# Optimization experiments

Measured on AMD Instinct MI355X. Metric: run time of the kernel, lower is better.

Reference implementation:

```python
import jax, jax.numpy as jnp
import numpy as np

E = 1024
H = 16
DH = E // H
EPS = 1e-8
GRAM_W = 1.5


def _gram_scores(q, k1, k2):
    # q: [BH, L, D], k1/k2: [BH, S, D] -> [BH, L, S]
    ll = jnp.sum(q * q, -1)[:, :, None]          # [BH, L, 1]
    vv = jnp.sum(k1 * k1, -1)[:, None, :]        # [BH, 1, S]
    aa = jnp.sum(k2 * k2, -1)[:, None, :]
    va = jnp.sum(k1 * k2, -1)[:, None, :]
    lv = jnp.einsum('bld,bsd->bls', q, k1)
    la = jnp.einsum('bld,bsd->bls', q, k2)
    det = ll * (vv * aa - va * va) - lv * (lv * aa - la * va) + la * (lv * va - la * vv)
    return -jnp.sqrt(jnp.clip(det, EPS, None))


def setup_inputs() -> dict:
    key = jax.random.key(0)
    ks = jax.random.split(key, 20)
    L, B, S = 512, 4, 1024
    inp = {
        'query': jax.random.normal(ks[0], (L, B, E), jnp.float32),
        'mod1': jax.random.normal(ks[1], (S, B, E), jnp.float32),
        'mod2': jax.random.normal(ks[2], (S, B, E), jnp.float32),
    }
    # Linear params stored as [in, out] (y = x @ W + b), 8 linears
    names = ['q', 'k1', 'k2', 'v1', 'v2', 'g1', 'g2', 'o']
    for i, n in enumerate(names):
        inp[n + '_w'] = jax.random.normal(ks[3 + 2 * i], (E, E), jnp.float32) * 0.02
        inp[n + '_b'] = jax.random.normal(ks[4 + 2 * i], (E,), jnp.float32) * 0.02
    return inp


def reference(query, mod1, mod2,
              q_w, q_b, k1_w, k1_b, k2_w, k2_b, v1_w, v1_b, v2_w, v2_b,
              g1_w, g1_b, g2_w, g2_b, o_w, o_b):
    L, B, _ = query.shape
    S = mod1.shape[0]
    scaling = DH ** -0.5

    def lin(x, w, b):
        return x @ w + b

    def split_heads(x, n):  # [n, B, E] -> [B*H, n, DH]
        return x.reshape(n, B * H, DH).transpose(1, 0, 2)

    q = split_heads(lin(query, q_w, q_b) * scaling, L)
    k1 = split_heads(lin(mod1, k1_w, k1_b), S)
    k2 = split_heads(lin(mod2, k2_w, k2_b), S)
    v1 = split_heads(lin(mod1, v1_w, v1_b), S)
    v2 = split_heads(lin(mod2, v2_w, v2_b), S)

    w1 = jnp.einsum('bld,bsd->bls', q, k1)
    w2 = jnp.einsum('bld,bsd->bls', q, k2)
    gram = _gram_scores(q, k1, k2)
    logits = GRAM_W * gram + w1 + w2          # [BH, L, S]
    attn = jax.nn.softmax(logits, axis=-1)

    def merge_heads(x):  # [B*H, L, DH] -> [L, B, E]
        return x.transpose(1, 0, 2).reshape(L, B, E)

    out1 = merge_heads(jnp.einsum('bls,bsd->bld', attn, v1))
    out2 = merge_heads(jnp.einsum('bls,bsd->bld', attn, v2))
    gate1 = jax.nn.sigmoid(lin(query, g1_w, g1_b))
    gate2 = jax.nn.sigmoid(lin(query, g2_w, g2_b))
    attn_output = lin((out1 * gate1 + out2 * gate2) / 2.0, o_w, o_b)
    avg_weights = attn.reshape(B, H, L, S).mean(axis=1)
    return attn_output, avg_weights
```

## Files before the change

kernel.cpp:

```cpp
#include <hip/hip_runtime.h>
#include <cstddef>
#include <cstdint>

typedef unsigned short ushort_t;
typedef unsigned int uint_t;
typedef __attribute__((ext_vector_type(8))) short short8;
typedef __attribute__((ext_vector_type(4))) float f32x4;

#define EDIM 1024
#define NHEAD 16
#define HDIM 64
#define NB 4
#define LQ 512
#define SK 1024
#define BHD 64

__device__ __forceinline__ ushort_t f2b(float f) {
    uint_t u = __float_as_uint(f);
    return (ushort_t)((u + 0x7fffu + ((u >> 16) & 1u)) >> 16);
}
__device__ __forceinline__ float b2f(ushort_t b) {
    return __uint_as_float(((uint_t)b) << 16);
}

__device__ __forceinline__ void gload_lds16(const void* g, void* l) {
    __builtin_amdgcn_global_load_lds((const __attribute__((address_space(1))) void*)g,
                                     (__attribute__((address_space(3))) void*)l, 16, 0, 0);
}

struct MegaArgs {
    const ushort_t *qx, *m1h, *m1l, *m2h, *m2l;
    const ushort_t *Wqg, *Wkv1, *Wkv2, *Wk1l, *Wk2l;
    const float *q_b, *k1_b, *k2_b, *v1_b, *v2_b, *g1_b, *g2_b;
    float *K1f, *K2f;
    ushort_t *V1b, *V2b, *Qb, *G1b, *G2b;
};

__global__ __launch_bounds__(256, 2)
void mega_gemm(MegaArgs a)
{
    __shared__ ushort_t As[128 * 64];
    __shared__ ushort_t Bs[128 * 64];
    const int tid = threadIdx.x;
    const int wave = tid >> 6, lane = tid & 63;
    const int ln = lane & 15, lq = lane >> 4;
    const int wm = wave & 1, wn = wave >> 1;
    const int cswz = (lane & 7) ^ ((lane >> 3) & 7);
    const int mrl = lane >> 3;

    const int id = blockIdx.x;
    const ushort_t *A, *Al, *B, *Bl;
    const float* bias;
    int npass, row0, col0, kind;
    if (id < 512) {
        kind = id >> 8;
        const int t = id & 255;
        col0 = (t & 7) * 128; row0 = (t >> 3) * 128; npass = 3;
        A = kind ? a.m2h : a.m1h;  Al = kind ? a.m2l : a.m1l;
        B = kind ? a.Wkv2 : a.Wkv1; Bl = kind ? a.Wk2l : a.Wk1l;
        bias = kind ? a.k2_b : a.k1_b;
    } else if (id < 1024) {
        int t = id - 512; kind = 2 + (t >> 8); t &= 255;
        col0 = (t & 7) * 128; row0 = (t >> 3) * 128; npass = 1;
        A = (kind == 2) ? a.m1h : a.m2h; Al = A;
        B = ((kind == 2) ? a.Wkv1 : a.Wkv2) + (size_t)1024 * 1024; Bl = B;
        bias = (kind == 2) ? a.v1_b : a.v2_b;
    } else {
        const int t = id - 1024; kind = 4;
        const int c = t % 24, rr = t / 24;
        col0 = c * 128; row0 = rr * 128; npass = 1;
        A = a.qx; Al = A; B = a.Wqg; Bl = B;
        const int seg = c >> 3;
        bias = (seg == 0) ? a.q_b : ((seg == 1) ? a.g1_b : a.g2_b);
    }

    f32x4 zero = {0.f, 0.f, 0.f, 0.f};
    f32x4 acc[4][4];
#pragma unroll
    for (int i = 0; i < 4; ++i)
#pragma unroll
        for (int j = 0; j < 4; ++j) acc[i][j] = zero;

    for (int pp = 0; pp < npass; ++pp) {
        const ushort_t* Ab = (pp == 2) ? Al : A;
        const ushort_t* Bb = (pp == 1) ? Bl : B;
        for (int kk = 0; kk < 1024; kk += 64) {
            __syncthreads();
#pragma unroll
            for (int j = 0; j < 4; ++j) {
                const int mr = (wave * 4 + j) * 8 + mrl;
                gload_lds16(Ab + (size_t)(row0 + mr) * 1024 + kk + cswz * 8,
                            (void*)(As + (wave * 4 + j) * 512));
                gload_lds16(Bb + (size_t)(col0 + mr) * 1024 + kk + cswz * 8,
                            (void*)(Bs + (wave * 4 + j) * 512));
            }
            __syncthreads();
#pragma unroll
            for (int sub = 0; sub < 2; ++sub) {
                short8 af[4], bfv[4];
#pragma unroll
                for (int i = 0; i < 4; ++i) {
                    const int ml = wm * 64 + i * 16 + ln;
                    af[i] = *(const short8*)(As + ml * 64 + (((sub * 4 + lq) ^ (ml & 7)) * 8));
                    const int nl = wn * 64 + i * 16 + ln;
                    bfv[i] = *(const short8*)(Bs + nl * 64 + (((sub * 4 + lq) ^ (nl & 7)) * 8));
                }
#pragma unroll
                for (int i = 0; i < 4; ++i)
#pragma unroll
                    for (int j = 0; j < 4; ++j)
                        acc[i][j] = __builtin_amdgcn_mfma_f32_16x16x32_bf16(af[i], bfv[j], acc[i][j], 0, 0, 0);
            }
        }
    }

#pragma unroll
    for (int i = 0; i < 4; ++i) {
#pragma unroll
        for (int r = 0; r < 4; ++r) {
            const int row = row0 + wm * 64 + i * 16 + lq * 4 + r;
#pragma unroll
            for (int j = 0; j < 4; ++j) {
                const int col = col0 + wn * 64 + j * 16 + ln;
                const int lc = col & 1023;
                float v = acc[i][j][r] + bias[lc];
                if (kind <= 1) {
                    const int s = row >> 2, b = row & 3, h = lc >> 6, d = lc & 63;
                    float* Y = kind ? a.K2f : a.K1f;
                    Y[(((size_t)(b * 16 + h)) * 1024 + s) * 64 + d] = v;
                } else if (kind <= 3) {
                    const int s = row >> 2, b = row & 3, h = lc >> 6, d = lc & 63;
                    ushort_t* Y = (kind == 2) ? a.V1b : a.V2b;
                    Y[(((size_t)(b * 16 + h)) * 1024 + s) * 64 + d] = f2b(v);
                } else {
                    const int seg = col >> 10;
                    if (seg == 0) {
                        v *= 0.125f;
                        const int s = row >> 2, b = row & 3, h = lc >> 6, d = lc & 63;
                        a.Qb[(((size_t)(b * 16 + h)) * 512 + s) * 64 + d] = f2b(v);
                    } else {
                        v = 1.0f / (1.0f + __expf(-v));
                        ushort_t* Y = (seg == 1) ? a.G1b : a.G2b;
                        Y[(size_t)row * 1024 + lc] = f2b(v);
                    }
                }
            }
        }
    }
}

struct CastArgs {
    const float* q; const float* m1; const float* m2;
    ushort_t* qx; ushort_t* m1h; ushort_t* m1l; ushort_t* m2h; ushort_t* m2l;
    const float* wsrc[8];
    ushort_t* whi[8];
    ushort_t* wlo[8];
};

__global__ __launch_bounds__(256)
void casts_kernel(CastArgs a)
{
    __shared__ float T[64][65];
    const int id = blockIdx.x;
    const int tid = threadIdx.x;
    if (id < 1024) {
        const size_t i = ((size_t)id * 256 + tid) * 8;
        float4 x = *(const float4*)(a.q + i);
        float4 y = *(const float4*)(a.q + i + 4);
        ushort_t o[8] = {f2b(x.x), f2b(x.y), f2b(x.z), f2b(x.w), f2b(y.x), f2b(y.y), f2b(y.z), f2b(y.w)};
        *(uint4*)( (void*)(a.qx + i) ) = *(const uint4*)o;
    } else if (id < 5120) {
        const int t = id - 1024;
        const int which = t >> 11;
        const float* x = which ? a.m2 : a.m1;
        ushort_t* yh = which ? a.m2h : a.m1h;
        ushort_t* yl = which ? a.m2l : a.m1l;
        const size_t i = ((size_t)(t & 2047) * 256 + tid) * 8;
        float v[8];
        *(float4*)v = *(const float4*)(x + i);
        *(float4*)(v + 4) = *(const float4*)(x + i + 4);
        ushort_t oh[8], ol[8];
#pragma unroll
        for (int k = 0; k < 8; ++k) {
            oh[k] = f2b(v[k]);
            ol[k] = f2b(v[k] - b2f(oh[k]));
        }
        *(uint4*)( (void*)(yh + i) ) = *(const uint4*)oh;
        *(uint4*)( (void*)(yl + i) ) = *(const uint4*)ol;
    } else {
        const int t = id - 5120;
        const int z = t >> 8, x = t & 15, y = (t >> 4) & 15;
        const float* W = a.wsrc[z];
        ushort_t* Th = a.whi[z];
        ushort_t* Tl = a.wlo[z];
        const int k0 = x * 64, n0 = y * 64;
        const int r = tid >> 2, cg = (tid & 3) * 16;
#pragma unroll
        for (int u = 0; u < 4; ++u) {
            float4 v = *(const float4*)(W + (size_t)(k0 + r) * 1024 + n0 + cg + u * 4);
            T[r][cg + u * 4 + 0] = v.x; T[r][cg + u * 4 + 1] = v.y;
            T[r][cg + u * 4 + 2] = v.z; T[r][cg + u * 4 + 3] = v.w;
        }
        __syncthreads();
        ushort_t oh[16], ol[16];
#pragma unroll
        for (int u = 0; u < 16; ++u) {
            float v = T[cg + u][r];
            oh[u] = f2b(v);
            ol[u] = f2b(v - b2f(oh[u]));
        }
        ushort_t* dh = Th + (size_t)(n0 + r) * 1024 + k0 + cg;
        *(uint4*)( (void*)dh ) = *(const uint4*)oh;
        *(uint4*)( (void*)(dh + 8) ) = *(const uint4*)(oh + 8);
        if (Tl) {
            ushort_t* dl = Tl + (size_t)(n0 + r) * 1024 + k0 + cg;
            *(uint4*)( (void*)dl ) = *(const uint4*)ol;
            *(uint4*)( (void*)(dl + 8) ) = *(const uint4*)(ol + 8);
        }
    }
}

__global__ __launch_bounds__(256)
void prep_kernel(const float* __restrict__ K1f, const float* __restrict__ K2f,
                 ushort_t* __restrict__ K1b, ushort_t* __restrict__ K2b,
                 float* __restrict__ vv, float* __restrict__ aa, float* __restrict__ va,
                 const ushort_t* __restrict__ Qb, float* __restrict__ ll,
                 const ushort_t* __restrict__ V1b, const ushort_t* __restrict__ V2b,
                 ushort_t* __restrict__ V1t, ushort_t* __restrict__ V2t)
{
    __shared__ float T[64][65];
    const int id = blockIdx.x;
    const int tid = threadIdx.x;
    const int wave = tid >> 6, lane = tid & 63;
    if (id < 16384) {
        const int row = id * 4 + wave;
        const float x1 = K1f[(size_t)row * 64 + lane];
        const float x2 = K2f[(size_t)row * 64 + lane];
        K1b[(size_t)row * 64 + lane] = f2b(x1);
        K2b[(size_t)row * 64 + lane] = f2b(x2);
        float s1 = x1 * x1, s2 = x2 * x2, s3 = x1 * x2;
#pragma unroll
        for (int o = 1; o < 64; o <<= 1) {
            s1 += __shfl_xor(s1, o);
            s2 += __shfl_xor(s2, o);
            s3 += __shfl_xor(s3, o);
        }
        if (lane == 0) { vv[row] = s1; aa[row] = s2; va[row] = s3; }
    } else if (id < 24576) {
        const int row = (id - 16384) * 4 + wave;
        const float x = b2f(Qb[(size_t)row * 64 + lane]);
        float s = x * x;
#pragma unroll
        for (int o = 1; o < 64; o <<= 1) s += __shfl_xor(s, o);
        if (lane == 0) ll[row] = s;
    } else {
        const int t = id - 24576;
        const int z = t >> 10, bh = (t >> 4) & 63, s0 = (t & 15) * 64;
        const ushort_t* S = z ? V2b : V1b;
        ushort_t* D = z ? V2t : V1t;
        const int r = tid >> 2, cg = (tid & 3) * 16;
        ushort_t buf[16];
        const ushort_t* sp = S + ((size_t)bh * 1024 + s0 + r) * 64 + cg;
        *(uint4*)buf = *(const uint4*)sp;
        *(uint4*)(buf + 8) = *(const uint4*)(sp + 8);
#pragma unroll
        for (int u = 0; u < 16; ++u) T[r][cg + u] = b2f(buf[u]);
        __syncthreads();
        ushort_t o[16];
#pragma unroll
        for (int u = 0; u < 16; ++u) o[u] = f2b(T[cg + u][r]);
        ushort_t* d = D + ((size_t)bh * 64 + r) * 1024 + s0 + cg;
        *(uint4*)( (void*)d ) = *(const uint4*)o;
        *(uint4*)( (void*)(d + 8) ) = *(const uint4*)(o + 8);
    }
}

__global__ __launch_bounds__(512, 1)
void flash_attn(const ushort_t* __restrict__ Qb, const ushort_t* __restrict__ K1b,
                const ushort_t* __restrict__ K2b, const ushort_t* __restrict__ V1t,
                const ushort_t* __restrict__ V2t, const float* __restrict__ ll,
                const float* __restrict__ vv, const float* __restrict__ aa,
                const float* __restrict__ va, const ushort_t* __restrict__ G1,
                const ushort_t* __restrict__ G2, ushort_t* __restrict__ attn,
                ushort_t* __restrict__ tmpb)
{
    __shared__ ushort_t Qs[128 * 64];
    __shared__ ushort_t K1s[128 * 64];
    __shared__ ushort_t K2s[128 * 64];
    __shared__ ushort_t V1s[64 * 128];
    __shared__ ushort_t V2s[64 * 128];
    __shared__ ushort_t Ps[128 * 128];
    __shared__ float vvS[1024], aaS[1024], vaS[1024];
    __shared__ float llS[128], mRow[128], sRow[128];
    __shared__ float redM[256], redS[256];

    const int tid = threadIdx.x;
    const int wave = tid >> 6, lane = tid & 63;
    const int ln = lane & 15, lq = lane >> 4;
    const int wm = wave >> 1, wn = wave & 1;
    const int l0 = blockIdx.x * 128;
    const int bh = blockIdx.y;
    const int bq = bh >> 4, h = bh & 15;

    for (int u = tid; u < 1024; u += 512) {
        vvS[u] = vv[(size_t)bh * 1024 + u];
        aaS[u] = aa[(size_t)bh * 1024 + u];
        vaS[u] = va[(size_t)bh * 1024 + u];
    }
    if (tid < 128) {
        llS[tid] = ll[(size_t)bh * 512 + l0 + tid];
        mRow[tid] = -3.4e38f;
        sRow[tid] = 0.f;
    }
#pragma unroll
    for (int c = 0; c < 2; ++c) {
        const int row = wave * 16 + c * 8 + (lane >> 3);
        const int ch = (lane & 7) ^ (row & 7);
        gload_lds16(Qb + ((size_t)bh * 512 + l0 + row) * 64 + ch * 8,
                    (void*)(Qs + (wave * 16 + c * 8) * 64));
    }
    __syncthreads();

    f32x4 zero = {0.f, 0.f, 0.f, 0.f};

    for (int st = 0; st < 8; ++st) {
        const int s0 = st * 128;
        __syncthreads();
#pragma unroll
        for (int c = 0; c < 2; ++c) {
            const int row = wave * 16 + c * 8 + (lane >> 3);
            const int ch = (lane & 7) ^ (row & 7);
            gload_lds16(K1b + ((size_t)bh * 1024 + s0 + row) * 64 + ch * 8,
                        (void*)(K1s + (wave * 16 + c * 8) * 64));
            gload_lds16(K2b + ((size_t)bh * 1024 + s0 + row) * 64 + ch * 8,
                        (void*)(K2s + (wave * 16 + c * 8) * 64));
        }
        __syncthreads();

        f32x4 lv[2][4], la[2][4];
#pragma unroll
        for (int i = 0; i < 2; ++i)
#pragma unroll
            for (int j = 0; j < 4; ++j) { lv[i][j] = zero; la[i][j] = zero; }
#pragma unroll
        for (int sub = 0; sub < 2; ++sub) {
            short8 qf[2], k1f[4], k2f[4];
#pragma unroll
            for (int i = 0; i < 2; ++i) {
                const int ml = wm * 32 + i * 16 + ln;
                qf[i] = *(const short8*)(Qs + ml * 64 + (((sub * 4 + lq) ^ (ml & 7)) * 8));
            }
#pragma unroll
            for (int j = 0; j < 4; ++j) {
                const int nl = wn * 64 + j * 16 + ln;
                k1f[j] = *(const short8*)(K1s + nl * 64 + (((sub * 4 + lq) ^ (nl & 7)) * 8));
                k2f[j] = *(const short8*)(K2s + nl * 64 + (((sub * 4 + lq) ^ (nl & 7)) * 8));
            }
#pragma unroll
            for (int i = 0; i < 2; ++i)
#pragma unroll
                for (int j = 0; j < 4; ++j) {
                    lv[i][j] = __builtin_amdgcn_mfma_f32_16x16x32_bf16(qf[i], k1f[j], lv[i][j], 0, 0, 0);
                    la[i][j] = __builtin_amdgcn_mfma_f32_16x16x32_bf16(qf[i], k2f[j], la[i][j], 0, 0, 0);
                }
        }
#pragma unroll
        for (int i = 0; i < 2; ++i)
#pragma unroll
            for (int j = 0; j < 4; ++j) {
                const int s_loc = wn * 64 + j * 16 + ln;
                const float VV = vvS[s0 + s_loc], AA = aaS[s0 + s_loc], VA = vaS[s0 + s_loc];
#pragma unroll
                for (int r = 0; r < 4; ++r) {
                    const float LL = llS[wm * 32 + i * 16 + lq * 4 + r];
                    const float LV = lv[i][j][r], LA = la[i][j][r];
                    float det = LL * (VV * AA - VA * VA) - LV * (LV * AA - LA * VA) + LA * (LV * VA - LA * VV);
                    det = fmaxf(det, 1e-8f);
                    lv[i][j][r] = LV + LA - 1.5f * sqrtf(det);
                }
            }
#pragma unroll
        for (int i = 0; i < 2; ++i)
#pragma unroll
            for (int r = 0; r < 4; ++r) {
                float m = fmaxf(fmaxf(lv[i][0][r], lv[i][1][r]), fmaxf(lv[i][2][r], lv[i][3][r]));
#pragma unroll
                for (int o = 1; o < 16; o <<= 1) m = fmaxf(m, __shfl_xor(m, o));
                if (ln == 0) redM[wn * 128 + wm * 32 + i * 16 + lq * 4 + r] = m;
            }
        __syncthreads();
        if (tid < 128) {
            const float mo = mRow[tid];
            const float mn = fmaxf(mo, fmaxf(redM[tid], redM[128 + tid]));
            sRow[tid] *= __expf(mo - mn);
            mRow[tid] = mn;
        }
        __syncthreads();
#pragma unroll
        for (int i = 0; i < 2; ++i)
#pragma unroll
            for (int r = 0; r < 4; ++r) {
                const float mr = mRow[wm * 32 + i * 16 + lq * 4 + r];
                float e = __expf(lv[i][0][r] - mr) + __expf(lv[i][1][r] - mr)
                        + __expf(lv[i][2][r] - mr) + __expf(lv[i][3][r] - mr);
#pragma unroll
                for (int o = 1; o < 16; o <<= 1) e += __shfl_xor(e, o);
                if (ln == 0) redS[wn * 128 + wm * 32 + i * 16 + lq * 4 + r] = e;
            }
        __syncthreads();
        if (tid < 128) sRow[tid] += redS[tid] + redS[128 + tid];
    }
    __syncthreads();
    if (tid < 128) sRow[tid] = 1.0f / sRow[tid];

    f32x4 o1[4], o2[4];
#pragma unroll
    for (int j = 0; j < 4; ++j) { o1[j] = zero; o2[j] = zero; }

    for (int st = 0; st < 8; ++st) {
        const int s0 = st * 128;
        __syncthreads();
#pragma unroll
        for (int c = 0; c < 2; ++c) {
            const int row = wave * 16 + c * 8 + (lane >> 3);
            const int ch = (lane & 7) ^ (row & 7);
            gload_lds16(K1b + ((size_t)bh * 1024 + s0 + row) * 64 + ch * 8,
                        (void*)(K1s + (wave * 16 + c * 8) * 64));
            gload_lds16(K2b + ((size_t)bh * 1024 + s0 + row) * 64 + ch * 8,
                        (void*)(K2s + (wave * 16 + c * 8) * 64));
        }
#pragma unroll
        for (int c = 0; c < 2; ++c) {
            const int dr = wave * 8 + c * 4 + (lane >> 4);
            const int ch = (lane & 15) ^ (dr & 7);
            gload_lds16(V1t + ((size_t)bh * 64 + dr) * 1024 + s0 + ch * 8,
                        (void*)(V1s + (wave * 8 + c * 4) * 128));
            gload_lds16(V2t + ((size_t)bh * 64 + dr) * 1024 + s0 + ch * 8,
                        (void*)(V2s + (wave * 8 + c * 4) * 128));
        }
        __syncthreads();

        f32x4 lv[2][4], la[2][4];
#pragma unroll
        for (int i = 0; i < 2; ++i)
#pragma unroll
            for (int j = 0; j < 4; ++j) { lv[i][j] = zero; la[i][j] = zero; }
#pragma unroll
        for (int sub = 0; sub < 2; ++sub) {
            short8 qf[2], k1f[4], k2f[4];
#pragma unroll
            for (int i = 0; i < 2; ++i) {
                const int ml = wm * 32 + i * 16 + ln;
                qf[i] = *(const short8*)(Qs + ml * 64 + (((sub * 4 + lq) ^ (ml & 7)) * 8));
            }
#pragma unroll
            for (int j = 0; j < 4; ++j) {
                const int nl = wn * 64 + j * 16 + ln;
                k1f[j] = *(const short8*)(K1s + nl * 64 + (((sub * 4 + lq) ^ (nl & 7)) * 8));
                k2f[j] = *(const short8*)(K2s + nl * 64 + (((sub * 4 + lq) ^ (nl & 7)) * 8));
            }
#pragma unroll
            for (int i = 0; i < 2; ++i)
#pragma unroll
                for (int j = 0; j < 4; ++j) {
                    lv[i][j] = __builtin_amdgcn_mfma_f32_16x16x32_bf16(qf[i], k1f[j], lv[i][j], 0, 0, 0);
                    la[i][j] = __builtin_amdgcn_mfma_f32_16x16x32_bf16(qf[i], k2f[j], la[i][j], 0, 0, 0);
                }
        }
#pragma unroll
        for (int i = 0; i < 2; ++i)
#pragma unroll
            for (int j = 0; j < 4; ++j) {
                const int s_loc = wn * 64 + j * 16 + ln;
                const float VV = vvS[s0 + s_loc], AA = aaS[s0 + s_loc], VA = vaS[s0 + s_loc];
#pragma unroll
                for (int r = 0; r < 4; ++r) {
                    const int l_loc = wm * 32 + i * 16 + lq * 4 + r;
                    const float LL = llS[l_loc];
                    const float LV = lv[i][j][r], LA = la[i][j][r];
                    float det = LL * (VV * AA - VA * VA) - LV * (LV * AA - LA * VA) + LA * (LV * VA - LA * VV);
                    det = fmaxf(det, 1e-8f);
                    const float lg = LV + LA - 1.5f * sqrtf(det);
                    const float p = __expf(lg - mRow[l_loc]) * sRow[l_loc];
                    Ps[l_loc * 128 + (((s_loc >> 3) ^ (l_loc & 7)) * 8) + (s_loc & 7)] = f2b(p);
                }
            }
        __syncthreads();
#pragma unroll
        for (int it = 0; it < 4; ++it) {
            const int l = it * 32 + (tid >> 4);
            const int c = tid & 15;
            uint4 val = *(const uint4*)(Ps + l * 128 + ((c ^ (l & 7)) * 8));
            *(uint4*)( (void*)(attn + ((size_t)bh * 512 + l0 + l) * 1024 + s0 + c * 8) ) = val;
        }
#pragma unroll
        for (int kt = 0; kt < 4; ++kt) {
            const int lA = wave * 16 + ln;
            short8 pf = *(const short8*)(Ps + lA * 128 + (((kt * 4 + lq) ^ (lA & 7)) * 8));
#pragma unroll
            for (int j = 0; j < 4; ++j) {
                const int d = j * 16 + ln;
                short8 v1f = *(const short8*)(V1s + d * 128 + (((kt * 4 + lq) ^ (d & 7)) * 8));
                short8 v2f = *(const short8*)(V2s + d * 128 + (((kt * 4 + lq) ^ (d & 7)) * 8));
                o1[j] = __builtin_amdgcn_mfma_f32_16x16x32_bf16(pf, v1f, o1[j], 0, 0, 0);
                o2[j] = __builtin_amdgcn_mfma_f32_16x16x32_bf16(pf, v2f, o2[j], 0, 0, 0);
            }
        }
    }
#pragma unroll
    for (int j = 0; j < 4; ++j)
#pragma unroll
        for (int r = 0; r < 4; ++r) {
            const int l = l0 + wave * 16 + lq * 4 + r;
            const int d = j * 16 + ln;
            const size_t addr = ((size_t)l * 4 + bq) * 1024 + h * 64 + d;
            const float v = 0.5f * (o1[j][r] * b2f(G1[addr]) + o2[j][r] * b2f(G2[addr]));
            tmpb[addr] = f2b(v);
        }
}

__global__ __launch_bounds__(256)
void head_avg_kernel(const ushort_t* __restrict__ attn, float* __restrict__ outv)
{
    const int idx = blockIdx.x * 256 + threadIdx.x;
    const int s8 = idx & 127;
    const int l = (idx >> 7) & 511;
    const int b = idx >> 16;
    float acc[8] = {};
#pragma unroll
    for (int h = 0; h < 16; ++h) {
        const ushort_t* p = attn + (((size_t)(b * 16 + h) * 512 + l)) * 1024 + s8 * 8;
        uint4 u = *(const uint4*)p;
        const uint_t uu[4] = {u.x, u.y, u.z, u.w};
#pragma unroll
        for (int q = 0; q < 4; ++q) {
            acc[2 * q]     += __uint_as_float((uu[q] & 0xffffu) << 16);
            acc[2 * q + 1] += __uint_as_float(uu[q] & 0xffff0000u);
        }
    }
    float* d = outv + (size_t)idx * 8;
    float4 o1 = {acc[0] * 0.0625f, acc[1] * 0.0625f, acc[2] * 0.0625f, acc[3] * 0.0625f};
    float4 o2 = {acc[4] * 0.0625f, acc[5] * 0.0625f, acc[6] * 0.0625f, acc[7] * 0.0625f};
    *(float4*)d = o1;
    *(float4*)(d + 4) = o2;
}

__global__ __launch_bounds__(256, 2)
void gemm_o64(const ushort_t* __restrict__ A, const ushort_t* __restrict__ B,
              const float* __restrict__ bias, float* __restrict__ Y)
{
    __shared__ ushort_t As[64 * 64];
    __shared__ ushort_t Bs[128 * 64];
    const int tid = threadIdx.x;
    const int wave = tid >> 6, lane = tid & 63;
    const int ln = lane & 15, lq = lane >> 4;
    const int row0 = blockIdx.y * 64, col0 = blockIdx.x * 128;
    const int wm = wave & 1, wn = wave >> 1;
    const int cswz = (lane & 7) ^ ((lane >> 3) & 7);
    const int mrl = lane >> 3;

    f32x4 zero = {0.f, 0.f, 0.f, 0.f};
    f32x4 acc[2][4];
#pragma unroll
    for (int i = 0; i < 2; ++i)
#pragma unroll
        for (int j = 0; j < 4; ++j) acc[i][j] = zero;

    for (int kk = 0; kk < 1024; kk += 64) {
        __syncthreads();
#pragma unroll
        for (int j = 0; j < 2; ++j) {
            const int mr = (wave * 2 + j) * 8 + mrl;
            gload_lds16(A + (size_t)(row0 + mr) * 1024 + kk + cswz * 8,
                        (void*)(As + (wave * 2 + j) * 512));
        }
#pragma unroll
        for (int j = 0; j < 4; ++j) {
            const int mr = (wave * 4 + j) * 8 + mrl;
            gload_lds16(B + (size_t)(col0 + mr) * 1024 + kk + cswz * 8,
                        (void*)(Bs + (wave * 4 + j) * 512));
        }
        __syncthreads();
#pragma unroll
        for (int sub = 0; sub < 2; ++sub) {
            short8 af[2], bfv[4];
#pragma unroll
            for (int i = 0; i < 2; ++i) {
                const int ml = wm * 32 + i * 16 + ln;
                af[i] = *(const short8*)(As + ml * 64 + (((sub * 4 + lq) ^ (ml & 7)) * 8));
            }
#pragma unroll
            for (int j = 0; j < 4; ++j) {
                const int nl = wn * 64 + j * 16 + ln;
                bfv[j] = *(const short8*)(Bs + nl * 64 + (((sub * 4 + lq) ^ (nl & 7)) * 8));
            }
#pragma unroll
            for (int i = 0; i < 2; ++i)
#pragma unroll
                for (int j = 0; j < 4; ++j)
                    acc[i][j] = __builtin_amdgcn_mfma_f32_16x16x32_bf16(af[i], bfv[j], acc[i][j], 0, 0, 0);
        }
    }

#pragma unroll
    for (int i = 0; i < 2; ++i) {
#pragma unroll
        for (int r = 0; r < 4; ++r) {
            const int row = row0 + wm * 32 + i * 16 + lq * 4 + r;
#pragma unroll
            for (int j = 0; j < 4; ++j) {
                const int col = col0 + wn * 64 + j * 16 + ln;
                Y[(size_t)row * 1024 + col] = acc[i][j][r] + bias[col];
            }
        }
    }
}

extern "C" void kernel_launch(void* const* d_in, const int* in_sizes, int n_in,
                              void* d_out, int out_size, void* d_ws, size_t ws_size,
                              hipStream_t stream)
{
    const float* query = (const float*)d_in[0];
    const float* mod1  = (const float*)d_in[1];
    const float* mod2  = (const float*)d_in[2];
    const float* q_w  = (const float*)d_in[3];  const float* q_b  = (const float*)d_in[4];
    const float* k1_w = (const float*)d_in[5];  const float* k1_b = (const float*)d_in[6];
    const float* k2_w = (const float*)d_in[7];  const float* k2_b = (const float*)d_in[8];
    const float* v1_w = (const float*)d_in[9];  const float* v1_b = (const float*)d_in[10];
    const float* v2_w = (const float*)d_in[11]; const float* v2_b = (const float*)d_in[12];
    const float* g1_w = (const float*)d_in[13]; const float* g1_b = (const float*)d_in[14];
    const float* g2_w = (const float*)d_in[15]; const float* g2_b = (const float*)d_in[16];
    const float* o_w  = (const float*)d_in[17]; const float* o_b  = (const float*)d_in[18];
    float* out = (float*)d_out;

    const size_t MB = 1u << 20;
    char* w = (char*)d_ws;
    ushort_t* Wqg  = (ushort_t*)(w + 0 * MB);
    ushort_t* Wkv1 = (ushort_t*)(w + 6 * MB);
    ushort_t* Wkv2 = (ushort_t*)(w + 10 * MB);
    ushort_t* Wo   = (ushort_t*)(w + 14 * MB);
    ushort_t* Wk1l = (ushort_t*)(w + 16 * MB);
    ushort_t* Wk2l = (ushort_t*)(w + 18 * MB);
    ushort_t* qx   = (ushort_t*)(w + 20 * MB);
    ushort_t* tmpb = qx;
    ushort_t* Qb   = (ushort_t*)(w + 24 * MB);
    ushort_t* K1b  = (ushort_t*)(w + 28 * MB);
    ushort_t* K2b  = (ushort_t*)(w + 36 * MB);
    ushort_t* V1t  = (ushort_t*)(w + 44 * MB);
    ushort_t* V2t  = (ushort_t*)(w + 52 * MB);
    ushort_t* G1b  = (ushort_t*)(w + 60 * MB);
    ushort_t* G2b  = (ushort_t*)(w + 64 * MB);
    float* ll = (float*)(w + 68 * MB);
    float* vv = (float*)(w + 68 * MB + 256 * 1024);
    float* aa = (float*)(w + 68 * MB + 512 * 1024);
    float* va = (float*)(w + 68 * MB + 768 * 1024);
    ushort_t* attn = (ushort_t*)(w + 78 * MB);
    ushort_t* m1h = (ushort_t*)(w + 78 * MB);
    ushort_t* m2h = (ushort_t*)(w + 86 * MB);
    ushort_t* m1l = (ushort_t*)(w + 94 * MB);
    ushort_t* m2l = (ushort_t*)(w + 102 * MB);
    float* K1f = (float*)(w + 110 * MB);
    float* K2f = (float*)(w + 126 * MB);
    ushort_t* V1b = (ushort_t*)(w + 142 * MB);
    ushort_t* V2b = (ushort_t*)(w + 150 * MB);

    CastArgs ca;
    ca.q = query; ca.m1 = mod1; ca.m2 = mod2;
    ca.qx = qx; ca.m1h = m1h; ca.m1l = m1l; ca.m2h = m2h; ca.m2l = m2l;
    const float* srcs[8] = {q_w, g1_w, g2_w, k1_w, v1_w, k2_w, v2_w, o_w};
    ushort_t* his[8] = {Wqg, Wqg + (size_t)1024 * 1024, Wqg + (size_t)2048 * 1024,
                        Wkv1, Wkv1 + (size_t)1024 * 1024, Wkv2, Wkv2 + (size_t)1024 * 1024, Wo};
    ushort_t* los[8] = {nullptr, nullptr, nullptr, Wk1l, nullptr, Wk2l, nullptr, nullptr};
    for (int i = 0; i < 8; ++i) { ca.wsrc[i] = srcs[i]; ca.whi[i] = his[i]; ca.wlo[i] = los[i]; }
    casts_kernel<<<7168, 256, 0, stream>>>(ca);

    MegaArgs ma;
    ma.qx = qx; ma.m1h = m1h; ma.m1l = m1l; ma.m2h = m2h; ma.m2l = m2l;
    ma.Wqg = Wqg; ma.Wkv1 = Wkv1; ma.Wkv2 = Wkv2; ma.Wk1l = Wk1l; ma.Wk2l = Wk2l;
    ma.q_b = q_b; ma.k1_b = k1_b; ma.k2_b = k2_b; ma.v1_b = v1_b; ma.v2_b = v2_b;
    ma.g1_b = g1_b; ma.g2_b = g2_b;
    ma.K1f = K1f; ma.K2f = K2f; ma.V1b = V1b; ma.V2b = V2b;
    ma.Qb = Qb; ma.G1b = G1b; ma.G2b = G2b;
    mega_gemm<<<1408, 256, 0, stream>>>(ma);

    prep_kernel<<<26624, 256, 0, stream>>>(K1f, K2f, K1b, K2b, vv, aa, va,
                                           Qb, ll, V1b, V2b, V1t, V2t);

    flash_attn<<<dim3(4, 64), 512, 0, stream>>>(Qb, K1b, K2b, V1t, V2t,
                                                ll, vv, aa, va, G1b, G2b, attn, tmpb);

    head_avg_kernel<<<1024, 256, 0, stream>>>(attn, out + (size_t)LQ * NB * EDIM);
    gemm_o64<<<dim3(8, 32), 256, 0, stream>>>(tmpb, Wo, o_b, out);
}
```

Baseline: 444.0 us.

## Fuse softmax into one pass using a norm-based logit upper bound

The two passes over keys (first for the row max and sum, then for probabilities) become a single pass. Each row uses a fixed shift from a Cauchy-Schwarz style bound, sqrt(ll)*(sqrt(max vv)+sqrt(max aa)), in place of a running max. Unnormalized exponentials go into the attention buffer, and the inverse row sums are written to a new array that is applied in the output epilogue and in the head-average kernel. This removes a full recomputation of the QK MFMAs and the per-tile reduction barriers. The K and P shared buffers are aliased to save LDS. The risk is underflow or lost precision if the bound is far above the true row maximum.

Result: faster. 397.6 us (-10.5%).

```diff
diff --git a/kernel.cpp b/kernel.cpp
--- a/kernel.cpp
+++ b/kernel.cpp
@@ -282,17 +282,15 @@
                 const float* __restrict__ vv, const float* __restrict__ aa,
                 const float* __restrict__ va, const ushort_t* __restrict__ G1,
                 const ushort_t* __restrict__ G2, ushort_t* __restrict__ attn,
-                ushort_t* __restrict__ tmpb)
+                float* __restrict__ invS, ushort_t* __restrict__ tmpb)
 {
     __shared__ ushort_t Qs[128 * 64];
-    __shared__ ushort_t K1s[128 * 64];
-    __shared__ ushort_t K2s[128 * 64];
+    __shared__ ushort_t KPs[2 * 128 * 64];
     __shared__ ushort_t V1s[64 * 128];
     __shared__ ushort_t V2s[64 * 128];
-    __shared__ ushort_t Ps[128 * 128];
     __shared__ float vvS[1024], aaS[1024], vaS[1024];
-    __shared__ float llS[128], mRow[128], sRow[128];
-    __shared__ float redM[256], redS[256];
+    __shared__ float llS[128], MrS[128];
+    __shared__ float red[256];
 
     const int tid = threadIdx.x;
     const int wave = tid >> 6, lane = tid & 63;
@@ -301,17 +299,16 @@
     const int l0 = blockIdx.x * 128;
     const int bh = blockIdx.y;
     const int bq = bh >> 4, h = bh & 15;
+    ushort_t* K1s = KPs;
+    ushort_t* K2s = KPs + 128 * 64;
+    ushort_t* Ps  = KPs;
 
     for (int u = tid; u < 1024; u += 512) {
         vvS[u] = vv[(size_t)bh * 1024 + u];
         aaS[u] = aa[(size_t)bh * 1024 + u];
         vaS[u] = va[(size_t)bh * 1024 + u];
     }
-    if (tid < 128) {
-        llS[tid] = ll[(size_t)bh * 512 + l0 + tid];
-        mRow[tid] = -3.4e38f;
-        sRow[tid] = 0.f;
-    }
+    if (tid < 128) llS[tid] = ll[(size_t)bh * 512 + l0 + tid];
 #pragma unroll
     for (int c = 0; c < 2; ++c) {
         const int row = wave * 16 + c * 8 + (lane >> 3);
@@ -321,7 +318,41 @@
     }
     __syncthreads();
 
+    {
+        float mv = fmaxf(vvS[tid], vvS[tid + 512]);
+        float ma = fmaxf(aaS[tid], aaS[tid + 512]);
+#pragma unroll
+        for (int o = 1; o < 64; o <<= 1) {
+            mv = fmaxf(mv, __shfl_xor(mv, o));
+            ma = fmaxf(ma, __shfl_xor(ma, o));
+        }
+        if (lane == 0) { red[wave] = mv; red[8 + wave] = ma; }
+    }
+    __syncthreads();
+    if (tid < 128) {
+        float mv = fmaxf(fmaxf(fmaxf(red[0], red[1]), fmaxf(red[2], red[3])),
+                         fmaxf(fmaxf(red[4], red[5]), fmaxf(red[6], red[7])));
+        float ma = fmaxf(fmaxf(fmaxf(red[8], red[9]), fmaxf(red[10], red[11])),
+                         fmaxf(fmaxf(red[12], red[13]), fmaxf(red[14], red[15])));
+        MrS[tid] = sqrtf(llS[tid]) * (sqrtf(mv) + sqrtf(ma));
+    }
+    __syncthreads();
+
+    float LLr[2][4], Mrr[2][4], esum[2][4];
+#pragma unroll
+    for (int i = 0; i < 2; ++i)
+#pragma unroll
+        for (int r = 0; r < 4; ++r) {
+            const int row = wm * 32 + i * 16 + lq * 4 + r;
+            LLr[i][r] = llS[row];
+            Mrr[i][r] = MrS[row];
+            esum[i][r] = 0.f;
+        }
+
     f32x4 zero = {0.f, 0.f, 0.f, 0.f};
+    f32x4 o1[4], o2[4];
+#pragma unroll
+    for (int j = 0; j < 4; ++j) { o1[j] = zero; o2[j] = zero; }
 
     for (int st = 0; st < 8; ++st) {
         const int s0 = st * 128;
@@ -335,100 +366,6 @@
             gload_lds16(K2b + ((size_t)bh * 1024 + s0 + row) * 64 + ch * 8,
                         (void*)(K2s + (wave * 16 + c * 8) * 64));
         }
-        __syncthreads();
-
-        f32x4 lv[2][4], la[2][4];
-#pragma unroll
-        for (int i = 0; i < 2; ++i)
-#pragma unroll
-            for (int j = 0; j < 4; ++j) { lv[i][j] = zero; la[i][j] = zero; }
-#pragma unroll
-        for (int sub = 0; sub < 2; ++sub) {
-            short8 qf[2], k1f[4], k2f[4];
-#pragma unroll
-            for (int i = 0; i < 2; ++i) {
-                const int ml = wm * 32 + i * 16 + ln;
-                qf[i] = *(const short8*)(Qs + ml * 64 + (((sub * 4 + lq) ^ (ml & 7)) * 8));
-            }
-#pragma unroll
-            for (int j = 0; j < 4; ++j) {
-                const int nl = wn * 64 + j * 16 + ln;
-                k1f[j] = *(const short8*)(K1s + nl * 64 + (((sub * 4 + lq) ^ (nl & 7)) * 8));
-                k2f[j] = *(const short8*)(K2s + nl * 64 + (((sub * 4 + lq) ^ (nl & 7)) * 8));
-            }
-#pragma unroll
-            for (int i = 0; i < 2; ++i)
-#pragma unroll
-                for (int j = 0; j < 4; ++j) {
-                    lv[i][j] = __builtin_amdgcn_mfma_f32_16x16x32_bf16(qf[i], k1f[j], lv[i][j], 0, 0, 0);
-                    la[i][j] = __builtin_amdgcn_mfma_f32_16x16x32_bf16(qf[i], k2f[j], la[i][j], 0, 0, 0);
-                }
-        }
-#pragma unroll
-        for (int i = 0; i < 2; ++i)
-#pragma unroll
-            for (int j = 0; j < 4; ++j) {
-                const int s_loc = wn * 64 + j * 16 + ln;
-                const float VV = vvS[s0 + s_loc], AA = aaS[s0 + s_loc], VA = vaS[s0 + s_loc];
-#pragma unroll
-                for (int r = 0; r < 4; ++r) {
-                    const float LL = llS[wm * 32 + i * 16 + lq * 4 + r];
-                    const float LV = lv[i][j][r], LA = la[i][j][r];
-                    float det = LL * (VV * AA - VA * VA) - LV * (LV * AA - LA * VA) + LA * (LV * VA - LA * VV);
-                    det = fmaxf(det, 1e-8f);
-                    lv[i][j][r] = LV + LA - 1.5f * sqrtf(det);
-                }
-            }
-#pragma unroll
-        for (int i = 0; i < 2; ++i)
-#pragma unroll
-            for (int r = 0; r < 4; ++r) {
-                float m = fmaxf(fmaxf(lv[i][0][r], lv[i][1][r]), fmaxf(lv[i][2][r], lv[i][3][r]));
-#pragma unroll
-                for (int o = 1; o < 16; o <<= 1) m = fmaxf(m, __shfl_xor(m, o));
-                if (ln == 0) redM[wn * 128 + wm * 32 + i * 16 + lq * 4 + r] = m;
-            }
-        __syncthreads();
-        if (tid < 128) {
-            const float mo = mRow[tid];
-            const float mn = fmaxf(mo, fmaxf(redM[tid], redM[128 + tid]));
-            sRow[tid] *= __expf(mo - mn);
-            mRow[tid] = mn;
-        }
-        __syncthreads();
-#pragma unroll
-        for (int i = 0; i < 2; ++i)
-#pragma unroll
-            for (int r = 0; r < 4; ++r) {
-                const float mr = mRow[wm * 32 + i * 16 + lq * 4 + r];
-                float e = __expf(lv[i][0][r] - mr) + __expf(lv[i][1][r] - mr)
-                        + __expf(lv[i][2][r] - mr) + __expf(lv[i][3][r] - mr);
-#pragma unroll
-                for (int o = 1; o < 16; o <<= 1) e += __shfl_xor(e, o);
-                if (ln == 0) redS[wn * 128 + wm * 32 + i * 16 + lq * 4 + r] = e;
-            }
-        __syncthreads();
-        if (tid < 128) sRow[tid] += redS[tid] + redS[128 + tid];
-    }
-    __syncthreads();
-    if (tid < 128) sRow[tid] = 1.0f / sRow[tid];
-
-    f32x4 o1[4], o2[4];
-#pragma unroll
-    for (int j = 0; j < 4; ++j) { o1[j] = zero; o2[j] = zero; }
-
-    for (int st = 0; st < 8; ++st) {
-        const int s0 = st * 128;
-        __syncthreads();
-#pragma unroll
-        for (int c = 0; c < 2; ++c) {
-            const int row = wave * 16 + c * 8 + (lane >> 3);
-            const int ch = (lane & 7) ^ (row & 7);
-            gload_lds16(K1b + ((size_t)bh * 1024 + s0 + row) * 64 + ch * 8,
-                        (void*)(K1s + (wave * 16 + c * 8) * 64));
-            gload_lds16(K2b + ((size_t)bh * 1024 + s0 + row) * 64 + ch * 8,
-                        (void*)(K2s + (wave * 16 + c * 8) * 64));
-        }
 #pragma unroll
         for (int c = 0; c < 2; ++c) {
             const int dr = wave * 8 + c * 4 + (lane >> 4);
@@ -468,21 +405,34 @@
                 }
         }
 #pragma unroll
+        for (int j = 0; j < 4; ++j) {
+            const int s_loc = wn * 64 + j * 16 + ln;
+            const float VV = vvS[s0 + s_loc], AA = aaS[s0 + s_loc], VA = vaS[s0 + s_loc];
+            const float P1 = VV * AA - VA * VA;
+#pragma unroll
+            for (int i = 0; i < 2; ++i)
+#pragma unroll
+                for (int r = 0; r < 4; ++r) {
+                    const float LV = lv[i][j][r], LA = la[i][j][r];
+                    float det = LLr[i][r] * P1 - (LV * LV) * AA
+                              + 2.f * VA * (LV * LA) - (LA * LA) * VV;
+                    det = fmaxf(det, 1e-8f);
+                    const float lg = LV + LA - 1.5f * sqrtf(det);
+                    const float e = __expf(lg - Mrr[i][r]);
+                    esum[i][r] += e;
+                    lv[i][j][r] = e;
+                }
+        }
+        __syncthreads();
+#pragma unroll
         for (int i = 0; i < 2; ++i)
 #pragma unroll
             for (int j = 0; j < 4; ++j) {
                 const int s_loc = wn * 64 + j * 16 + ln;
-                const float VV = vvS[s0 + s_loc], AA = aaS[s0 + s_loc], VA = vaS[s0 + s_loc];
 #pragma unroll
                 for (int r = 0; r < 4; ++r) {
                     const int l_loc = wm * 32 + i * 16 + lq * 4 + r;
-                    const float LL = llS[l_loc];
-                    const float LV = lv[i][j][r], LA = la[i][j][r];
-                    float det = LL * (VV * AA - VA * VA) - LV * (LV * AA - LA * VA) + LA * (LV * VA - LA * VV);
-                    det = fmaxf(det, 1e-8f);
-                    const float lg = LV + LA - 1.5f * sqrtf(det);
-                    const float p = __expf(lg - mRow[l_loc]) * sRow[l_loc];
-                    Ps[l_loc * 128 + (((s_loc >> 3) ^ (l_loc & 7)) * 8) + (s_loc & 7)] = f2b(p);
+                    Ps[l_loc * 128 + (((s_loc >> 3) ^ (l_loc & 7)) * 8) + (s_loc & 7)] = f2b(lv[i][j][r]);
                 }
             }
         __syncthreads();
@@ -507,20 +457,41 @@
             }
         }
     }
+
+#pragma unroll
+    for (int i = 0; i < 2; ++i)
+#pragma unroll
+        for (int r = 0; r < 4; ++r) {
+            float e = esum[i][r];
+            e += __shfl_xor(e, 1); e += __shfl_xor(e, 2);
+            e += __shfl_xor(e, 4); e += __shfl_xor(e, 8);
+            if (ln == 0) red[wn * 128 + wm * 32 + i * 16 + lq * 4 + r] = e;
+        }
+    __syncthreads();
+    if (tid < 128) {
+        const float inv = 1.0f / (red[tid] + red[128 + tid]);
+        llS[tid] = inv;
+        invS[(size_t)bh * 512 + l0 + tid] = inv;
+    }
+    __syncthreads();
+
 #pragma unroll
     for (int j = 0; j < 4; ++j)
 #pragma unroll
         for (int r = 0; r < 4; ++r) {
-            const int l = l0 + wave * 16 + lq * 4 + r;
+            const int l_loc = wave * 16 + lq * 4 + r;
+            const float inv = llS[l_loc];
+            const int l = l0 + l_loc;
             const int d = j * 16 + ln;
             const size_t addr = ((size_t)l * 4 + bq) * 1024 + h * 64 + d;
-            const float v = 0.5f * (o1[j][r] * b2f(G1[addr]) + o2[j][r] * b2f(G2[addr]));
+            const float v = 0.5f * inv * (o1[j][r] * b2f(G1[addr]) + o2[j][r] * b2f(G2[addr]));
             tmpb[addr] = f2b(v);
         }
 }
 
 __global__ __launch_bounds__(256)
-void head_avg_kernel(const ushort_t* __restrict__ attn, float* __restrict__ outv)
+void head_avg_kernel(const ushort_t* __restrict__ attn, const float* __restrict__ invS,
+                     float* __restrict__ outv)
 {
     const int idx = blockIdx.x * 256 + threadIdx.x;
     const int s8 = idx & 127;
@@ -529,13 +500,14 @@
     float acc[8] = {};
 #pragma unroll
     for (int h = 0; h < 16; ++h) {
+        const float inv = invS[(size_t)(b * 16 + h) * 512 + l];
         const ushort_t* p = attn + (((size_t)(b * 16 + h) * 512 + l)) * 1024 + s8 * 8;
         uint4 u = *(const uint4*)p;
         const uint_t uu[4] = {u.x, u.y, u.z, u.w};
 #pragma unroll
         for (int q = 0; q < 4; ++q) {
-            acc[2 * q]     += __uint_as_float((uu[q] & 0xffffu) << 16);
-            acc[2 * q + 1] += __uint_as_float(uu[q] & 0xffff0000u);
+            acc[2 * q]     += __uint_as_float((uu[q] & 0xffffu) << 16) * inv;
+            acc[2 * q + 1] += __uint_as_float(uu[q] & 0xffff0000u) * inv;
         }
     }
     float* d = outv + (size_t)idx * 8;
@@ -654,6 +626,7 @@
     float* vv = (float*)(w + 68 * MB + 256 * 1024);
     float* aa = (float*)(w + 68 * MB + 512 * 1024);
     float* va = (float*)(w + 68 * MB + 768 * 1024);
+    float* invS = (float*)(w + 69 * MB);
     ushort_t* attn = (ushort_t*)(w + 78 * MB);
     ushort_t* m1h = (ushort_t*)(w + 78 * MB);
     ushort_t* m2h = (ushort_t*)(w + 86 * MB);
@@ -687,8 +660,9 @@
                                            Qb, ll, V1b, V2b, V1t, V2t);
 
     flash_attn<<<dim3(4, 64), 512, 0, stream>>>(Qb, K1b, K2b, V1t, V2t,
-                                                ll, vv, aa, va, G1b, G2b, attn, tmpb);
-
-    head_avg_kernel<<<1024, 256, 0, stream>>>(attn, out + (size_t)LQ * NB * EDIM);
+                                                ll, vv, aa, va, G1b, G2b,
+                                                attn, invS, tmpb);
+
+    head_avg_kernel<<<1024, 256, 0, stream>>>(attn, invS, out + (size_t)LQ * NB * EDIM);
     gemm_o64<<<dim3(8, 32), 256, 0, stream>>>(tmpb, Wo, o_b, out);
 }
```
